# Performance work log

Measured on AMD Instinct MI355X. Metric: run time of the kernel, lower is better.

The kernel has to match this reference:

```python
import jax, jax.numpy as jnp
import numpy as np

B, S, DIN, DIM, H = 2, 2304, 1024, 1024, 16
HEAD_DIM = DIM // H            # 64
ROT_DIM = HEAD_DIM             # partial_rotary_factor = 1
BASE = 10000.0
EPS = 1e-6


def setup_inputs() -> dict:
    key = jax.random.key(0)
    ks = jax.random.split(key, 6)
    return {
        "input": jax.random.normal(ks[0], (B, S, DIN), dtype=jnp.float32),
        "qkv_w": jax.random.normal(ks[1], (3 * DIM, DIN), dtype=jnp.float32) * 0.02,
        "qkv_b": jnp.zeros((3 * DIM,), dtype=jnp.float32),
        "q_scale": jnp.ones((DIM,), dtype=jnp.float32),
        "k_scale": jnp.ones((DIM,), dtype=jnp.float32),
        "proj_w": jax.random.normal(ks[2], (DIN, DIM), dtype=jnp.float32) * 0.02,
        "proj_b": jnp.zeros((DIN,), dtype=jnp.float32),
        "height": 48,
        "width": 48,
    }


def _rms_norm(x, scale):
    # RMSNorm over the full inner dim (QKNorm), learned scale
    var = jnp.mean(x * x, axis=-1, keepdims=True)
    return x * jax.lax.rsqrt(var + EPS) * scale


def _rope_1d(x, pos):
    # x: (b, n, h, d_ax), pos: (n,) float; rotate_half-style RoPE
    d = x.shape[-1]
    inv_freq = 1.0 / (BASE ** (jnp.arange(0, d, 2, dtype=jnp.float32) / d))  # (d/2,)
    ang = pos[:, None] * inv_freq                                            # (n, d/2)
    cos = jnp.concatenate([jnp.cos(ang), jnp.cos(ang)], axis=-1)[None, :, None, :]
    sin = jnp.concatenate([jnp.sin(ang), jnp.sin(ang)], axis=-1)[None, :, None, :]
    x1, x2 = jnp.split(x, 2, axis=-1)
    rot = jnp.concatenate([-x2, x1], axis=-1)
    return x * cos + rot * sin


def _rope_2d(x, height, width):
    # axial 2D RoPE: first half of rotary dims keyed by row, second half by col
    n = height * width
    idx = jnp.arange(n, dtype=jnp.float32)
    rows = jnp.floor(idx / width)
    cols = jnp.mod(idx, width)
    half = ROT_DIM // 2
    x_r = _rope_1d(x[..., :half], rows)
    x_c = _rope_1d(x[..., half:ROT_DIM], cols)
    return jnp.concatenate([x_r, x_c, x[..., ROT_DIM:]], axis=-1)


def reference(input, qkv_w, qkv_b, q_scale, k_scale, proj_w, proj_b, height, width):
    b, n, _ = input.shape
    qkv = input @ qkv_w.T + qkv_b                       # (b, n, 3*dim)
    q, k, v = jnp.split(qkv, 3, axis=-1)
    q = _rms_norm(q, q_scale)
    k = _rms_norm(k, k_scale)
    # (b, n, h, d)
    q = q.reshape(b, n, H, HEAD_DIM)
    k = k.reshape(b, n, H, HEAD_DIM)
    v = v.reshape(b, n, H, HEAD_DIM)
    q = _rope_2d(q, height, width)
    k = _rope_2d(k, height, width)
    scale = HEAD_DIM ** (-0.5)
    # (b, h, q, k)
    scores = jnp.einsum("bqhd,bkhd->bhqk", q, k) * scale
    attn = jax.nn.softmax(scores, axis=-1)
    out = jnp.einsum("bhqk,bkhd->bqhd", attn, v)        # (b, n, h, d)
    out = out.reshape(b, n, DIM)
    return out @ proj_w.T + proj_b
```

## Files before the change

### kernel.cpp

```cpp
#include <hip/hip_runtime.h>
#include <math.h>

#define BB   2
#define SS   2304
#define DINC 1024
#define DIMC 1024
#define HH   16
#define HD   64

typedef _Float16 half_t;
typedef __attribute__((ext_vector_type(4))) _Float16 half4;
typedef __attribute__((ext_vector_type(8))) _Float16 half8;
typedef __attribute__((ext_vector_type(4))) float    f32x4;

#define LOG2E 1.44269504088896340736f
#define EXP2(x) __builtin_amdgcn_exp2f(x)

__device__ __forceinline__ half4 lo4(half8 x) { return (half4){x[0], x[1], x[2], x[3]}; }
__device__ __forceinline__ half4 hi4(half8 x) { return (half4){x[4], x[5], x[6], x[7]}; }

#define GLOAD_LDS16(gp, lp)                                                     \
    __builtin_amdgcn_global_load_lds(                                           \
        (const __attribute__((address_space(1))) void*)(gp),                    \
        (__attribute__((address_space(3))) void*)(lp), 16, 0, 0)

template<int RB>
__global__ __launch_bounds__(256)
void convert_tile_f16(const float* __restrict__ src, half_t* __restrict__ dst, int K)
{
    constexpr int EPT = RB * 32 / 256;
    const int mb = blockIdx.x;
    const int kb = blockIdx.y;
    const int t  = threadIdx.x;
    const int e0 = t * EPT;
    const int mm = e0 >> 5;
    const int kk = e0 & 31;
    const float* sp = src + (size_t)(mb * RB + mm) * K + kb * 32 + kk;
    half_t*      dp = dst + ((size_t)mb * (K >> 5) + kb) * (RB * 32) + mm * 32 + kk;
    #pragma unroll
    for (int g = 0; g < EPT / 4; ++g) {
        float4 v = *(const float4*)(sp + 4 * g);
        dp[4 * g + 0] = (half_t)v.x; dp[4 * g + 1] = (half_t)v.y;
        dp[4 * g + 2] = (half_t)v.z; dp[4 * g + 3] = (half_t)v.w;
    }
}

template<int BN, bool OUT_HALF>
__global__ __launch_bounds__(256)
void gemm_mfma(const half_t* __restrict__ Ah, const half_t* __restrict__ Bh,
               const float* __restrict__ bias, void* __restrict__ Cout,
               int M, int N, int K)
{
    constexpr int MT = (BN == 128) ? 4 : 2;
    constexpr int NT = 4;
    const int KB = K >> 5;
    __shared__ half_t As[8192];
    __shared__ half_t Bs[2 * BN * 32];

    const int t    = threadIdx.x;
    const int w    = t >> 6;
    const int lane = t & 63;
    const int l15  = lane & 15, quad = lane >> 4;
    const int wr   = (BN == 128) ? (w >> 1) : w;
    const int wc   = (BN == 128) ? (w & 1) : 0;
    const int mb   = blockIdx.y, nb = blockIdx.x;

    f32x4 acc[MT][NT];
    #pragma unroll
    for (int mt = 0; mt < MT; ++mt)
        #pragma unroll
        for (int nt = 0; nt < NT; ++nt) acc[mt][nt] = (f32x4){0.f, 0.f, 0.f, 0.f};

    const half_t* atile = Ah + (size_t)mb * KB * 4096;
    const half_t* btile = Bh + (size_t)nb * KB * (BN * 32);

    for (int kb = 0; kb < KB; kb += 2) {
        #pragma unroll
        for (int u = 0; u < 2; ++u) {
            const half_t* at = atile + (size_t)(kb + u) * 4096;
            const half_t* bt = btile + (size_t)(kb + u) * (BN * 32);
            #pragma unroll
            for (int v = 0; v < 2; ++v) {
                const int ch = w * 2 + v;
                GLOAD_LDS16(at + ch * 512 + lane * 8, As + u * 4096 + ch * 512);
            }
            if (BN == 128) {
                #pragma unroll
                for (int v = 0; v < 2; ++v) {
                    const int ch = w * 2 + v;
                    GLOAD_LDS16(bt + ch * 512 + lane * 8, Bs + u * 4096 + ch * 512);
                }
            } else {
                GLOAD_LDS16(bt + w * 512 + lane * 8, Bs + u * (BN * 32) + w * 512);
            }
        }
        __syncthreads();

        #pragma unroll
        for (int u = 0; u < 2; ++u) {
            half8 af[MT], bf[NT];
            #pragma unroll
            for (int mt = 0; mt < MT; ++mt)
                af[mt] = *(const half8*)(As + u * 4096
                                         + (wr * (MT * 16) + mt * 16 + l15) * 32 + quad * 8);
            #pragma unroll
            for (int nt = 0; nt < NT; ++nt)
                bf[nt] = *(const half8*)(Bs + u * (BN * 32)
                                         + (wc * 64 + nt * 16 + l15) * 32 + quad * 8);
            #pragma unroll
            for (int mt = 0; mt < MT; ++mt)
                #pragma unroll
                for (int nt = 0; nt < NT; ++nt)
                    acc[mt][nt] = __builtin_amdgcn_mfma_f32_16x16x32_f16(
                        af[mt], bf[nt], acc[mt][nt], 0, 0, 0);
        }
        __syncthreads();
    }

    const int bm = mb * 128, bn = nb * BN;
    #pragma unroll
    for (int nt = 0; nt < NT; ++nt) {
        const int n  = bn + wc * 64 + nt * 16 + l15;
        const float bv = bias[n];
        #pragma unroll
        for (int mt = 0; mt < MT; ++mt) {
            const int m0 = bm + wr * (MT * 16) + mt * 16 + quad * 4;
            #pragma unroll
            for (int rg = 0; rg < 4; ++rg) {
                const float v = acc[mt][nt][rg] + bv;
                if (OUT_HALF) ((half_t*)Cout)[(size_t)(m0 + rg) * N + n] = (half_t)v;
                else          ((float*) Cout)[(size_t)(m0 + rg) * N + n] = v;
            }
        }
    }
}

__global__ __launch_bounds__(256)
void normrope_v6(half_t* __restrict__ qkvh, const float* __restrict__ q_scale,
                 const float* __restrict__ k_scale, const int* __restrict__ wptr,
                 half_t* __restrict__ Kf, half_t* __restrict__ Vf)
{
    const int token = blockIdx.x;
    const int s     = token % SS;
    const int b     = token / SS;
    const int w     = *wptr;
    const int t     = threadIdx.x;
    const float rowp = (float)(s / w);
    const float colp = (float)(s % w);

    half_t* base = qkvh + (size_t)token * 3072;

    const int fr = s >> 5;
    const int jt = (s >> 4) & 1;

    {
        half4 v4 = *(const half4*)(base + 2048 + 4 * t);
        const int dabs0 = 4 * t;
        const int h  = dabs0 >> 6;
        const int vq = (s & 15) >> 2;
        const int vi = s & 3;
        half_t* vdst = Vf + ((size_t)(b * HH + h) * 72 + fr) * 2048 + jt * 1024;
        #pragma unroll
        for (int ii = 0; ii < 4; ++ii) {
            const int d   = (dabs0 + ii) & 63;
            const int dt  = d >> 4;
            vdst[(size_t)(dt >> 1) * 512 + ((d & 15) + 16 * vq) * 8 + (dt & 1) * 4 + vi]
                = v4[ii];
        }
    }

    __shared__ float buf[DIMC];
    __shared__ float red[4];

    const int km = s & 15;

    #pragma unroll
    for (int sel = 0; sel < 2; ++sel) {
        half_t* row = base + sel * DIMC;
        const float* scp = sel ? k_scale : q_scale;

        half4 xh = *(const half4*)(row + 4 * t);
        float x0 = (float)xh[0], x1 = (float)xh[1], x2 = (float)xh[2], x3 = (float)xh[3];
        float ss = x0 * x0 + x1 * x1 + x2 * x2 + x3 * x3;
        #pragma unroll
        for (int o = 32; o >= 1; o >>= 1) ss += __shfl_xor(ss, o);
        if ((t & 63) == 0) red[t >> 6] = ss;
        __syncthreads();

        const float rinv = rsqrtf((red[0] + red[1] + red[2] + red[3]) * (1.0f / DIMC) + 1e-6f);
        float4 g = *(const float4*)(scp + 4 * t);
        buf[4 * t + 0] = x0 * rinv * g.x;
        buf[4 * t + 1] = x1 * rinv * g.y;
        buf[4 * t + 2] = x2 * rinv * g.z;
        buf[4 * t + 3] = x3 * rinv * g.w;
        __syncthreads();

        const float qsc = sel ? 1.0f : (0.125f * LOG2E);

        #pragma unroll
        for (int pp = 0; pp < 2; ++pp) {
            const int p = t + pp * 256;
            const int h = p >> 5;
            const int r = p & 31;
            const int j = r & 15;
            const float pos = (r < 16) ? rowp : colp;
            const int d1 = (r < 16) ? j : (32 + j);
            const int d2 = d1 + 16;
            const float freq = exp2f((float)j * -0.83048202372f);
            const float ang  = pos * freq;
            float sn, cs;
            __sincosf(ang, &sn, &cs);
            const float a1 = buf[h * HD + d1], a2 = buf[h * HD + d2];
            const float o1 = (a1 * cs - a2 * sn) * qsc;
            const float o2 = (a2 * cs + a1 * sn) * qsc;
            if (sel == 0) {
                row[h * HD + d1] = (half_t)o1;
                row[h * HD + d2] = (half_t)o2;
            } else {
                half_t* kdst = Kf + ((size_t)(b * HH + h) * 72 + fr) * 2048 + jt * 1024;
                kdst[(size_t)(d1 >> 5) * 512 + (km + 16 * ((d1 & 31) >> 3)) * 8 + (d1 & 7)]
                    = (half_t)o1;
                kdst[(size_t)(d2 >> 5) * 512 + (km + 16 * ((d2 & 31) >> 3)) * 8 + (d2 & 7)]
                    = (half_t)o2;
            }
        }
        __syncthreads();
    }
}

__global__ __launch_bounds__(256, 4)
void flash_attn_mfma6(const half_t* __restrict__ qkvh, const half_t* __restrict__ Kf,
                      const half_t* __restrict__ Vf, half_t* __restrict__ attn_h)
{
    const int flat = blockIdx.x;
    const int xcd  = flat & 7;
    const int jj   = flat >> 3;
    const int bh   = xcd * 4 + (jj / 36);
    const int qtb  = jj % 36;
    const int b    = bh >> 4, h = bh & 15;
    const int t    = threadIdx.x;
    const int w    = t >> 6;
    const int jt   = w & 1;
    const int qh   = w >> 1;
    const int lane = t & 63;
    const int l15  = lane & 15, quad = lane >> 4;

    const size_t tb = (size_t)b * SS;
    const int q0 = qtb * 64;

    __shared__ float mlb[4][32][2];
    __shared__ float Ob[2][64][33];

    half8 qf[2][2];
    #pragma unroll
    for (int qt = 0; qt < 2; ++qt)
        #pragma unroll
        for (int dt2 = 0; dt2 < 2; ++dt2)
            qf[qt][dt2] = *(const half8*)(qkvh + (tb + q0 + qh * 32 + qt * 16 + l15) * 3072
                                          + h * HD + dt2 * 32 + quad * 8);

    f32x4 acc[4][2];
    float m_i[2], l_i[2];
    #pragma unroll
    for (int qt = 0; qt < 2; ++qt) {
        m_i[qt] = -INFINITY; l_i[qt] = 0.f;
        #pragma unroll
        for (int dt = 0; dt < 4; ++dt) acc[dt][qt] = (f32x4){0.f, 0.f, 0.f, 0.f};
    }

    const half_t* kpl = Kf + (size_t)bh * 72 * 2048 + jt * 1024 + lane * 8;
    const half_t* vpl = Vf + (size_t)bh * 72 * 2048 + jt * 1024 + lane * 8;

    auto step = [&](half8 kf0, half8 kf1, half8 v01, half8 v23) {
        half4 vf[4] = {lo4(v01), hi4(v01), lo4(v23), hi4(v23)};
        f32x4 sc[2];
        #pragma unroll
        for (int qt = 0; qt < 2; ++qt) {
            sc[qt] = (f32x4){0.f, 0.f, 0.f, 0.f};
            sc[qt] = __builtin_amdgcn_mfma_f32_16x16x32_f16(kf0, qf[qt][0], sc[qt], 0, 0, 0);
            sc[qt] = __builtin_amdgcn_mfma_f32_16x16x32_f16(kf1, qf[qt][1], sc[qt], 0, 0, 0);
        }
        half4 pf[2];
        #pragma unroll
        for (int qt = 0; qt < 2; ++qt) {
            float mx = fmaxf(fmaxf(sc[qt][0], sc[qt][1]), fmaxf(sc[qt][2], sc[qt][3]));
            mx = fmaxf(mx, __shfl_xor(mx, 16));
            mx = fmaxf(mx, __shfl_xor(mx, 32));
            if (__any(mx > m_i[qt])) {
                const float mn = fmaxf(m_i[qt], mx);
                const float alpha = EXP2(m_i[qt] - mn);
                m_i[qt] = mn;
                l_i[qt] *= alpha;
                #pragma unroll
                for (int dt = 0; dt < 4; ++dt) acc[dt][qt] *= alpha;
            }
            const float m = m_i[qt];
            const float p0 = EXP2(sc[qt][0] - m);
            const float p1 = EXP2(sc[qt][1] - m);
            const float p2 = EXP2(sc[qt][2] - m);
            const float p3 = EXP2(sc[qt][3] - m);
            l_i[qt] += (p0 + p1) + (p2 + p3);
            pf[qt] = (half4){(half_t)p0, (half_t)p1, (half_t)p2, (half_t)p3};
        }
        #pragma unroll
        for (int dt = 0; dt < 4; ++dt)
            #pragma unroll
            for (int qt = 0; qt < 2; ++qt)
                acc[dt][qt] = __builtin_amdgcn_mfma_f32_16x16x16f16(
                    vf[dt], pf[qt], acc[dt][qt], 0, 0, 0);
    };

    half8 kA0 = *(const half8*)(kpl);
    half8 kA1 = *(const half8*)(kpl + 512);
    half8 vA0 = *(const half8*)(vpl);
    half8 vA1 = *(const half8*)(vpl + 512);

    for (int fr2 = 0; fr2 < 36; ++fr2) {
        const int fr = fr2 * 2;
        const half_t* kB = kpl + (size_t)(fr + 1) * 2048;
        const half_t* vB = vpl + (size_t)(fr + 1) * 2048;
        half8 kB0 = *(const half8*)(kB);
        half8 kB1 = *(const half8*)(kB + 512);
        half8 vB0 = *(const half8*)(vB);
        half8 vB1 = *(const half8*)(vB + 512);

        step(kA0, kA1, vA0, vA1);

        if (fr + 2 < 72) {
            const half_t* kA = kpl + (size_t)(fr + 2) * 2048;
            const half_t* vA = vpl + (size_t)(fr + 2) * 2048;
            kA0 = *(const half8*)(kA);
            kA1 = *(const half8*)(kA + 512);
            vA0 = *(const half8*)(vA);
            vA1 = *(const half8*)(vA + 512);
        }

        step(kB0, kB1, vB0, vB1);
    }

    #pragma unroll
    for (int qt = 0; qt < 2; ++qt) {
        float lq = l_i[qt];
        lq += __shfl_xor(lq, 16);
        lq += __shfl_xor(lq, 32);
        if (quad == 0) {
            mlb[w][qt * 16 + l15][0] = m_i[qt];
            mlb[w][qt * 16 + l15][1] = lq;
        }
    }
    __syncthreads();

    float fac[2];
    #pragma unroll
    for (int qt = 0; qt < 2; ++qt) {
        const int q = qt * 16 + l15;
        const float m0 = mlb[qh * 2 + 0][q][0], m1 = mlb[qh * 2 + 1][q][0];
        const float M  = fmaxf(m0, m1);
        const float L  = mlb[qh * 2 + 0][q][1] * EXP2(m0 - M)
                       + mlb[qh * 2 + 1][q][1] * EXP2(m1 - M);
        fac[qt] = EXP2(m_i[qt] - M) / L;
    }

    #pragma unroll
    for (int ph = 0; ph < 2; ++ph) {
        if (jt == ph) {
            #pragma unroll
            for (int dt = 0; dt < 4; ++dt)
                #pragma unroll
                for (int qt = 0; qt < 2; ++qt)
                    #pragma unroll
                    for (int rg = 0; rg < 4; ++rg) {
                        const int d = dt * 16 + quad * 4 + rg;
                        const int q = qt * 16 + l15;
                        const float v = acc[dt][qt][rg] * fac[qt];
                        if (ph == 0) Ob[qh][d][q] = v;
                        else         Ob[qh][d][q] += v;
                    }
        }
        __syncthreads();
    }

    {
        const int q   = t >> 2;
        const int ds  = (t & 3) * 16;
        const int qh2 = q >> 5, qq = q & 31;
        const size_t mrow = tb + q0 + q;
        const int mb2 = (int)(mrow >> 7);
        const int mm  = (int)(mrow & 127);
        #pragma unroll
        for (int g = 0; g < 4; ++g) {
            const int dd = ds + 4 * g;
            const int kb2 = (h * HD + dd) >> 5;
            const int kk  = dd & 31;
            half4 o;
            o[0] = (half_t)Ob[qh2][dd + 0][qq];
            o[1] = (half_t)Ob[qh2][dd + 1][qq];
            o[2] = (half_t)Ob[qh2][dd + 2][qq];
            o[3] = (half_t)Ob[qh2][dd + 3][qq];
            *(half4*)(attn_h + ((size_t)mb2 * 32 + kb2) * 4096 + mm * 32 + kk) = o;
        }
    }
}

extern "C" void kernel_launch(void* const* d_in, const int* in_sizes, int n_in,
                              void* d_out, int out_size, void* d_ws, size_t ws_size,
                              hipStream_t stream)
{
    const float* input   = (const float*)d_in[0];
    const float* qkv_w   = (const float*)d_in[1];
    const float* qkv_b   = (const float*)d_in[2];
    const float* q_scale = (const float*)d_in[3];
    const float* k_scale = (const float*)d_in[4];
    const float* proj_w  = (const float*)d_in[5];
    const float* proj_b  = (const float*)d_in[6];
    const int*   width   = (const int*)d_in[8];
    float* out = (float*)d_out;

    half_t* qkvh   = (half_t*)d_ws;
    half_t* attn_h = qkvh   + (size_t)4608 * 3072;
    half_t* Vf     = attn_h + (size_t)4608 * 1024;
    half_t* Ah     = Vf     + (size_t)32 * 72 * 2048;
    half_t* Bh1    = Ah     + (size_t)4608 * 1024;
    half_t* Bh2    = Bh1    + (size_t)3072 * 1024;
    half_t* Kf     = Ah;

    const int M = BB * SS;

    convert_tile_f16<128><<<dim3(M / 128, DINC / 32),        256, 0, stream>>>(input,  Ah,  DINC);
    convert_tile_f16<128><<<dim3(3 * DIMC / 128, DINC / 32), 256, 0, stream>>>(qkv_w, Bh1, DINC);
    convert_tile_f16<64><<<dim3(DINC / 64, DIMC / 32),       256, 0, stream>>>(proj_w, Bh2, DIMC);

    gemm_mfma<128, true><<<dim3(3 * DIMC / 128, M / 128), 256, 0, stream>>>(
        Ah, Bh1, qkv_b, qkvh, M, 3 * DIMC, DINC);

    normrope_v6<<<M, 256, 0, stream>>>(qkvh, q_scale, k_scale, width, Kf, Vf);

    flash_attn_mfma6<<<dim3(SS / 64 * BB * HH), 256, 0, stream>>>(qkvh, Kf, Vf, attn_h);

    gemm_mfma<64, false><<<dim3(DINC / 64, M / 128), 256, 0, stream>>>(
        attn_h, Bh2, proj_b, out, M, DINC, DIMC);
}
```

Baseline: 271.0 us.

## Process two key tiles per softmax step and use 16x16x32 MFMA for PV

The K/V pre-layout in the norm/RoPE kernel is reorganised so each attention step handles 32 keys per wave. The score max, rescale and exp work is amortised over two 16-key tiles, and the PV product uses the wider 16x16x32 f16 MFMA in place of the 16x16x16 one. The norm/RoPE kernel now runs Q and K normalisation in parallel within a single 512-thread block, with no sequential loop. The cost is more live registers in the attention step, which may pressure occupancy at launch bound 4.

```diff
diff --git a/kernel.cpp b/kernel.cpp
--- a/kernel.cpp
+++ b/kernel.cpp
@@ -15,9 +15,6 @@
 
 #define LOG2E 1.44269504088896340736f
 #define EXP2(x) __builtin_amdgcn_exp2f(x)
-
-__device__ __forceinline__ half4 lo4(half8 x) { return (half4){x[0], x[1], x[2], x[3]}; }
-__device__ __forceinline__ half4 hi4(half8 x) { return (half4){x[4], x[5], x[6], x[7]}; }
 
 #define GLOAD_LDS16(gp, lp)                                                     \
     __builtin_amdgcn_global_load_lds(                                           \
@@ -135,8 +132,8 @@
     }
 }
 
-__global__ __launch_bounds__(256)
-void normrope_v6(half_t* __restrict__ qkvh, const float* __restrict__ q_scale,
+__global__ __launch_bounds__(512)
+void normrope_v7(half_t* __restrict__ qkvh, const float* __restrict__ q_scale,
                  const float* __restrict__ k_scale, const int* __restrict__ wptr,
                  half_t* __restrict__ Kf, half_t* __restrict__ Vf)
 {
@@ -150,86 +147,84 @@
 
     half_t* base = qkvh + (size_t)token * 3072;
 
-    const int fr = s >> 5;
-    const int jt = (s >> 4) & 1;
+    const int g36 = s >> 6;
+    const int jt  = (s >> 4) & 1;
+    const int kp_ = ((s >> 5) & 1) * 16 + (s & 15);
 
     {
-        half4 v4 = *(const half4*)(base + 2048 + 4 * t);
-        const int dabs0 = 4 * t;
-        const int h  = dabs0 >> 6;
-        const int vq = (s & 15) >> 2;
-        const int vi = s & 3;
-        half_t* vdst = Vf + ((size_t)(b * HH + h) * 72 + fr) * 2048 + jt * 1024;
-        #pragma unroll
-        for (int ii = 0; ii < 4; ++ii) {
-            const int d   = (dabs0 + ii) & 63;
-            const int dt  = d >> 4;
-            vdst[(size_t)(dt >> 1) * 512 + ((d & 15) + 16 * vq) * 8 + (dt & 1) * 4 + vi]
-                = v4[ii];
-        }
-    }
-
-    __shared__ float buf[DIMC];
-    __shared__ float red[4];
-
-    const int km = s & 15;
-
-    #pragma unroll
-    for (int sel = 0; sel < 2; ++sel) {
-        half_t* row = base + sel * DIMC;
-        const float* scp = sel ? k_scale : q_scale;
-
-        half4 xh = *(const half4*)(row + 4 * t);
-        float x0 = (float)xh[0], x1 = (float)xh[1], x2 = (float)xh[2], x3 = (float)xh[3];
-        float ss = x0 * x0 + x1 * x1 + x2 * x2 + x3 * x3;
-        #pragma unroll
-        for (int o = 32; o >= 1; o >>= 1) ss += __shfl_xor(ss, o);
-        if ((t & 63) == 0) red[t >> 6] = ss;
-        __syncthreads();
-
-        const float rinv = rsqrtf((red[0] + red[1] + red[2] + red[3]) * (1.0f / DIMC) + 1e-6f);
-        float4 g = *(const float4*)(scp + 4 * t);
-        buf[4 * t + 0] = x0 * rinv * g.x;
-        buf[4 * t + 1] = x1 * rinv * g.y;
-        buf[4 * t + 2] = x2 * rinv * g.z;
-        buf[4 * t + 3] = x3 * rinv * g.w;
-        __syncthreads();
-
-        const float qsc = sel ? 1.0f : (0.125f * LOG2E);
-
-        #pragma unroll
-        for (int pp = 0; pp < 2; ++pp) {
-            const int p = t + pp * 256;
-            const int h = p >> 5;
-            const int r = p & 31;
-            const int j = r & 15;
-            const float pos = (r < 16) ? rowp : colp;
-            const int d1 = (r < 16) ? j : (32 + j);
-            const int d2 = d1 + 16;
-            const float freq = exp2f((float)j * -0.83048202372f);
-            const float ang  = pos * freq;
-            float sn, cs;
-            __sincosf(ang, &sn, &cs);
-            const float a1 = buf[h * HD + d1], a2 = buf[h * HD + d2];
-            const float o1 = (a1 * cs - a2 * sn) * qsc;
-            const float o2 = (a2 * cs + a1 * sn) * qsc;
-            if (sel == 0) {
-                row[h * HD + d1] = (half_t)o1;
-                row[h * HD + d2] = (half_t)o2;
-            } else {
-                half_t* kdst = Kf + ((size_t)(b * HH + h) * 72 + fr) * 2048 + jt * 1024;
-                kdst[(size_t)(d1 >> 5) * 512 + (km + 16 * ((d1 & 31) >> 3)) * 8 + (d1 & 7)]
-                    = (half_t)o1;
-                kdst[(size_t)(d2 >> 5) * 512 + (km + 16 * ((d2 & 31) >> 3)) * 8 + (d2 & 7)]
-                    = (half_t)o2;
-            }
-        }
-        __syncthreads();
+        const int e0 = 2 * t;
+        const int kq = kp_ >> 3, ki = kp_ & 7;
+        #pragma unroll
+        for (int ii = 0; ii < 2; ++ii) {
+            const int e = e0 + ii;
+            const int h = e >> 6;
+            const int d = e & 63;
+            half_t* vdst = Vf + (((size_t)(b * HH + h) * 36 + g36) * 2 + jt) * 2048;
+            vdst[(size_t)(d >> 4) * 512 + ((d & 15) + 16 * kq) * 8 + ki] = base[2048 + e];
+        }
+    }
+
+    __shared__ float buf[2][DIMC];
+    __shared__ float red[8];
+
+    const int sel = t >> 8;
+    const int tl  = t & 255;
+    half_t* row = base + sel * DIMC;
+    const float* scp = sel ? k_scale : q_scale;
+
+    half4 xh = *(const half4*)(row + 4 * tl);
+    float x0 = (float)xh[0], x1 = (float)xh[1], x2 = (float)xh[2], x3 = (float)xh[3];
+    float ss = x0 * x0 + x1 * x1 + x2 * x2 + x3 * x3;
+    #pragma unroll
+    for (int o = 32; o >= 1; o >>= 1) ss += __shfl_xor(ss, o);
+    if ((tl & 63) == 0) red[sel * 4 + (tl >> 6)] = ss;
+    __syncthreads();
+
+    const float rinv = rsqrtf((red[sel * 4 + 0] + red[sel * 4 + 1]
+                             + red[sel * 4 + 2] + red[sel * 4 + 3]) * (1.0f / DIMC) + 1e-6f);
+    float4 g = *(const float4*)(scp + 4 * tl);
+    buf[sel][4 * tl + 0] = x0 * rinv * g.x;
+    buf[sel][4 * tl + 1] = x1 * rinv * g.y;
+    buf[sel][4 * tl + 2] = x2 * rinv * g.z;
+    buf[sel][4 * tl + 3] = x3 * rinv * g.w;
+    __syncthreads();
+
+    const float qsc = sel ? 1.0f : (0.125f * LOG2E);
+    const int ktile = (kp_ >> 2) & 1;
+    const int km    = ((kp_ >> 3) << 2) + (kp_ & 3);
+
+    #pragma unroll
+    for (int pp = 0; pp < 2; ++pp) {
+        const int p = tl + pp * 256;
+        const int h = p >> 5;
+        const int r = p & 31;
+        const int j = r & 15;
+        const float pos = (r < 16) ? rowp : colp;
+        const int d1 = (r < 16) ? j : (32 + j);
+        const int d2 = d1 + 16;
+        const float freq = exp2f((float)j * -0.83048202372f);
+        const float ang  = pos * freq;
+        float sn, cs;
+        __sincosf(ang, &sn, &cs);
+        const float a1 = buf[sel][h * HD + d1], a2 = buf[sel][h * HD + d2];
+        const float o1 = (a1 * cs - a2 * sn) * qsc;
+        const float o2 = (a2 * cs + a1 * sn) * qsc;
+        if (sel == 0) {
+            row[h * HD + d1] = (half_t)o1;
+            row[h * HD + d2] = (half_t)o2;
+        } else {
+            half_t* kdst = Kf + (((size_t)(b * HH + h) * 36 + g36) * 2 + jt) * 2048
+                         + ktile * 1024;
+            kdst[(size_t)(d1 >> 5) * 512 + (km + 16 * ((d1 & 31) >> 3)) * 8 + (d1 & 7)]
+                = (half_t)o1;
+            kdst[(size_t)(d2 >> 5) * 512 + (km + 16 * ((d2 & 31) >> 3)) * 8 + (d2 & 7)]
+                = (half_t)o2;
+        }
     }
 }
 
 __global__ __launch_bounds__(256, 4)
-void flash_attn_mfma6(const half_t* __restrict__ qkvh, const half_t* __restrict__ Kf,
+void flash_attn_mfma7(const half_t* __restrict__ qkvh, const half_t* __restrict__ Kf,
                       const half_t* __restrict__ Vf, half_t* __restrict__ attn_h)
 {
     const int flat = blockIdx.x;
@@ -268,22 +263,28 @@
         for (int dt = 0; dt < 4; ++dt) acc[dt][qt] = (f32x4){0.f, 0.f, 0.f, 0.f};
     }
 
-    const half_t* kpl = Kf + (size_t)bh * 72 * 2048 + jt * 1024 + lane * 8;
-    const half_t* vpl = Vf + (size_t)bh * 72 * 2048 + jt * 1024 + lane * 8;
-
-    auto step = [&](half8 kf0, half8 kf1, half8 v01, half8 v23) {
-        half4 vf[4] = {lo4(v01), hi4(v01), lo4(v23), hi4(v23)};
-        f32x4 sc[2];
+    const half_t* kpl = Kf + (((size_t)bh * 36) * 2 + jt) * 2048 + lane * 8;
+    const half_t* vpl = Vf + (((size_t)bh * 36) * 2 + jt) * 2048 + lane * 8;
+
+    auto step = [&](half8 kA0, half8 kA1, half8 kB0, half8 kB1,
+                    half8 v0, half8 v1, half8 v2, half8 v3) {
+        f32x4 scA[2], scB[2];
         #pragma unroll
         for (int qt = 0; qt < 2; ++qt) {
-            sc[qt] = (f32x4){0.f, 0.f, 0.f, 0.f};
-            sc[qt] = __builtin_amdgcn_mfma_f32_16x16x32_f16(kf0, qf[qt][0], sc[qt], 0, 0, 0);
-            sc[qt] = __builtin_amdgcn_mfma_f32_16x16x32_f16(kf1, qf[qt][1], sc[qt], 0, 0, 0);
-        }
-        half4 pf[2];
+            scA[qt] = (f32x4){0.f, 0.f, 0.f, 0.f};
+            scB[qt] = (f32x4){0.f, 0.f, 0.f, 0.f};
+            scA[qt] = __builtin_amdgcn_mfma_f32_16x16x32_f16(kA0, qf[qt][0], scA[qt], 0, 0, 0);
+            scA[qt] = __builtin_amdgcn_mfma_f32_16x16x32_f16(kA1, qf[qt][1], scA[qt], 0, 0, 0);
+            scB[qt] = __builtin_amdgcn_mfma_f32_16x16x32_f16(kB0, qf[qt][0], scB[qt], 0, 0, 0);
+            scB[qt] = __builtin_amdgcn_mfma_f32_16x16x32_f16(kB1, qf[qt][1], scB[qt], 0, 0, 0);
+        }
+        half8 pf[2];
         #pragma unroll
         for (int qt = 0; qt < 2; ++qt) {
-            float mx = fmaxf(fmaxf(sc[qt][0], sc[qt][1]), fmaxf(sc[qt][2], sc[qt][3]));
+            float mx = fmaxf(fmaxf(fmaxf(scA[qt][0], scA[qt][1]),
+                                   fmaxf(scA[qt][2], scA[qt][3])),
+                             fmaxf(fmaxf(scB[qt][0], scB[qt][1]),
+                                   fmaxf(scB[qt][2], scB[qt][3])));
             mx = fmaxf(mx, __shfl_xor(mx, 16));
             mx = fmaxf(mx, __shfl_xor(mx, 32));
             if (__any(mx > m_i[qt])) {
@@ -295,47 +296,65 @@
                 for (int dt = 0; dt < 4; ++dt) acc[dt][qt] *= alpha;
             }
             const float m = m_i[qt];
-            const float p0 = EXP2(sc[qt][0] - m);
-            const float p1 = EXP2(sc[qt][1] - m);
-            const float p2 = EXP2(sc[qt][2] - m);
-            const float p3 = EXP2(sc[qt][3] - m);
-            l_i[qt] += (p0 + p1) + (p2 + p3);
-            pf[qt] = (half4){(half_t)p0, (half_t)p1, (half_t)p2, (half_t)p3};
-        }
+            const float pA0 = EXP2(scA[qt][0] - m);
+            const float pA1 = EXP2(scA[qt][1] - m);
+            const float pA2 = EXP2(scA[qt][2] - m);
+            const float pA3 = EXP2(scA[qt][3] - m);
+            const float pB0 = EXP2(scB[qt][0] - m);
+            const float pB1 = EXP2(scB[qt][1] - m);
+            const float pB2 = EXP2(scB[qt][2] - m);
+            const float pB3 = EXP2(scB[qt][3] - m);
+            l_i[qt] += ((pA0 + pA1) + (pA2 + pA3)) + ((pB0 + pB1) + (pB2 + pB3));
+            pf[qt] = (half8){(half_t)pA0, (half_t)pA1, (half_t)pA2, (half_t)pA3,
+                             (half_t)pB0, (half_t)pB1, (half_t)pB2, (half_t)pB3};
+        }
+        half8 vf[4] = {v0, v1, v2, v3};
         #pragma unroll
         for (int dt = 0; dt < 4; ++dt)
             #pragma unroll
             for (int qt = 0; qt < 2; ++qt)
-                acc[dt][qt] = __builtin_amdgcn_mfma_f32_16x16x16f16(
+                acc[dt][qt] = __builtin_amdgcn_mfma_f32_16x16x32_f16(
                     vf[dt], pf[qt], acc[dt][qt], 0, 0, 0);
     };
 
     half8 kA0 = *(const half8*)(kpl);
     half8 kA1 = *(const half8*)(kpl + 512);
-    half8 vA0 = *(const half8*)(vpl);
-    half8 vA1 = *(const half8*)(vpl + 512);
-
-    for (int fr2 = 0; fr2 < 36; ++fr2) {
-        const int fr = fr2 * 2;
-        const half_t* kB = kpl + (size_t)(fr + 1) * 2048;
-        const half_t* vB = vpl + (size_t)(fr + 1) * 2048;
-        half8 kB0 = *(const half8*)(kB);
-        half8 kB1 = *(const half8*)(kB + 512);
-        half8 vB0 = *(const half8*)(vB);
-        half8 vB1 = *(const half8*)(vB + 512);
-
-        step(kA0, kA1, vA0, vA1);
-
-        if (fr + 2 < 72) {
-            const half_t* kA = kpl + (size_t)(fr + 2) * 2048;
-            const half_t* vA = vpl + (size_t)(fr + 2) * 2048;
-            kA0 = *(const half8*)(kA);
-            kA1 = *(const half8*)(kA + 512);
-            vA0 = *(const half8*)(vA);
-            vA1 = *(const half8*)(vA + 512);
-        }
-
-        step(kB0, kB1, vB0, vB1);
+    half8 kB0 = *(const half8*)(kpl + 1024);
+    half8 kB1 = *(const half8*)(kpl + 1536);
+    half8 va0 = *(const half8*)(vpl);
+    half8 va1 = *(const half8*)(vpl + 512);
+    half8 va2 = *(const half8*)(vpl + 1024);
+    half8 va3 = *(const half8*)(vpl + 1536);
+
+    for (int g2 = 0; g2 < 18; ++g2) {
+        const int g = g2 * 2;
+        const half_t* kN = kpl + (size_t)(g + 1) * 4096;
+        const half_t* vN = vpl + (size_t)(g + 1) * 4096;
+        half8 nk0 = *(const half8*)(kN);
+        half8 nk1 = *(const half8*)(kN + 512);
+        half8 nk2 = *(const half8*)(kN + 1024);
+        half8 nk3 = *(const half8*)(kN + 1536);
+        half8 nv0 = *(const half8*)(vN);
+        half8 nv1 = *(const half8*)(vN + 512);
+        half8 nv2 = *(const half8*)(vN + 1024);
+        half8 nv3 = *(const half8*)(vN + 1536);
+
+        step(kA0, kA1, kB0, kB1, va0, va1, va2, va3);
+
+        if (g + 2 < 36) {
+            const half_t* kM = kpl + (size_t)(g + 2) * 4096;
+            const half_t* vM = vpl + (size_t)(g + 2) * 4096;
+            kA0 = *(const half8*)(kM);
+            kA1 = *(const half8*)(kM + 512);
+            kB0 = *(const half8*)(kM + 1024);
+            kB1 = *(const half8*)(kM + 1536);
+            va0 = *(const half8*)(vM);
+            va1 = *(const half8*)(vM + 512);
+            va2 = *(const half8*)(vM + 1024);
+            va3 = *(const half8*)(vM + 1536);
+        }
+
+        step(nk0, nk1, nk2, nk3, nv0, nv1, nv2, nv3);
     }
 
     #pragma unroll
@@ -419,7 +438,7 @@
     half_t* qkvh   = (half_t*)d_ws;
     half_t* attn_h = qkvh   + (size_t)4608 * 3072;
     half_t* Vf     = attn_h + (size_t)4608 * 1024;
-    half_t* Ah     = Vf     + (size_t)32 * 72 * 2048;
+    half_t* Ah     = Vf     + (size_t)32 * 36 * 2 * 2048;
     half_t* Bh1    = Ah     + (size_t)4608 * 1024;
     half_t* Bh2    = Bh1    + (size_t)3072 * 1024;
     half_t* Kf     = Ah;
@@ -433,9 +452,9 @@
     gemm_mfma<128, true><<<dim3(3 * DIMC / 128, M / 128), 256, 0, stream>>>(
         Ah, Bh1, qkv_b, qkvh, M, 3 * DIMC, DINC);
 
-    normrope_v6<<<M, 256, 0, stream>>>(qkvh, q_scale, k_scale, width, Kf, Vf);
-
-    flash_attn_mfma6<<<dim3(SS / 64 * BB * HH), 256, 0, stream>>>(qkvh, Kf, Vf, attn_h);
+    normrope_v7<<<M, 512, 0, stream>>>(qkvh, q_scale, k_scale, width, Kf, Vf);
+
+    flash_attn_mfma7<<<dim3(SS / 64 * BB * HH), 256, 0, stream>>>(qkvh, Kf, Vf, attn_h);
 
     gemm_mfma<64, false><<<dim3(DINC / 64, M / 128), 256, 0, stream>>>(
         attn_h, Bh2, proj_b, out, M, DINC, DIMC);
```

Measured after the change: 325.0 us. 1.2x slower.

## Process two key frames per online-softmax step and split K/V prefetch

Applied to the files above, without the earlier changes.

The attention inner loop now computes scores for two 16-key frames together and runs a single max/rescale update over 32 keys instead of one per frame. This halves the cross-lane shuffles and conditional rescales. The next K fragments are prefetched right after the QK MFMAs, and the next V fragments after the PV MFMAs, so loads overlap with the softmax and matmul work. The cost is more live registers (two score sets and four K/V fragment pairs), which could lower occupancy under the 4-block launch bound.

```diff
diff --git a/kernel.cpp b/kernel.cpp
--- a/kernel.cpp
+++ b/kernel.cpp
@@ -229,7 +229,7 @@
 }
 
 __global__ __launch_bounds__(256, 4)
-void flash_attn_mfma6(const half_t* __restrict__ qkvh, const half_t* __restrict__ Kf,
+void flash_attn_mfma8(const half_t* __restrict__ qkvh, const half_t* __restrict__ Kf,
                       const half_t* __restrict__ Vf, half_t* __restrict__ attn_h)
 {
     const int flat = blockIdx.x;
@@ -271,19 +271,42 @@
     const half_t* kpl = Kf + (size_t)bh * 72 * 2048 + jt * 1024 + lane * 8;
     const half_t* vpl = Vf + (size_t)bh * 72 * 2048 + jt * 1024 + lane * 8;
 
-    auto step = [&](half8 kf0, half8 kf1, half8 v01, half8 v23) {
-        half4 vf[4] = {lo4(v01), hi4(v01), lo4(v23), hi4(v23)};
-        f32x4 sc[2];
+    half8 kA0 = *(const half8*)(kpl);
+    half8 kA1 = *(const half8*)(kpl + 512);
+    half8 kB0 = *(const half8*)(kpl + 2048);
+    half8 kB1 = *(const half8*)(kpl + 2560);
+    half8 vA0 = *(const half8*)(vpl);
+    half8 vA1 = *(const half8*)(vpl + 512);
+    half8 vB0 = *(const half8*)(vpl + 2048);
+    half8 vB1 = *(const half8*)(vpl + 2560);
+
+    for (int p = 0; p < 36; ++p) {
+        f32x4 scA[2], scB[2];
         #pragma unroll
         for (int qt = 0; qt < 2; ++qt) {
-            sc[qt] = (f32x4){0.f, 0.f, 0.f, 0.f};
-            sc[qt] = __builtin_amdgcn_mfma_f32_16x16x32_f16(kf0, qf[qt][0], sc[qt], 0, 0, 0);
-            sc[qt] = __builtin_amdgcn_mfma_f32_16x16x32_f16(kf1, qf[qt][1], sc[qt], 0, 0, 0);
-        }
-        half4 pf[2];
+            scA[qt] = (f32x4){0.f, 0.f, 0.f, 0.f};
+            scA[qt] = __builtin_amdgcn_mfma_f32_16x16x32_f16(kA0, qf[qt][0], scA[qt], 0, 0, 0);
+            scA[qt] = __builtin_amdgcn_mfma_f32_16x16x32_f16(kA1, qf[qt][1], scA[qt], 0, 0, 0);
+            scB[qt] = (f32x4){0.f, 0.f, 0.f, 0.f};
+            scB[qt] = __builtin_amdgcn_mfma_f32_16x16x32_f16(kB0, qf[qt][0], scB[qt], 0, 0, 0);
+            scB[qt] = __builtin_amdgcn_mfma_f32_16x16x32_f16(kB1, qf[qt][1], scB[qt], 0, 0, 0);
+        }
+
+        if (p + 1 < 36) {
+            const half_t* kN = kpl + (size_t)(p + 1) * 4096;
+            kA0 = *(const half8*)(kN);
+            kA1 = *(const half8*)(kN + 512);
+            kB0 = *(const half8*)(kN + 2048);
+            kB1 = *(const half8*)(kN + 2560);
+        }
+
+        half4 pfA[2], pfB[2];
         #pragma unroll
         for (int qt = 0; qt < 2; ++qt) {
-            float mx = fmaxf(fmaxf(sc[qt][0], sc[qt][1]), fmaxf(sc[qt][2], sc[qt][3]));
+            float mx = fmaxf(fmaxf(fmaxf(scA[qt][0], scA[qt][1]),
+                                   fmaxf(scA[qt][2], scA[qt][3])),
+                             fmaxf(fmaxf(scB[qt][0], scB[qt][1]),
+                                   fmaxf(scB[qt][2], scB[qt][3])));
             mx = fmaxf(mx, __shfl_xor(mx, 16));
             mx = fmaxf(mx, __shfl_xor(mx, 32));
             if (__any(mx > m_i[qt])) {
@@ -295,47 +318,38 @@
                 for (int dt = 0; dt < 4; ++dt) acc[dt][qt] *= alpha;
             }
             const float m = m_i[qt];
-            const float p0 = EXP2(sc[qt][0] - m);
-            const float p1 = EXP2(sc[qt][1] - m);
-            const float p2 = EXP2(sc[qt][2] - m);
-            const float p3 = EXP2(sc[qt][3] - m);
-            l_i[qt] += (p0 + p1) + (p2 + p3);
-            pf[qt] = (half4){(half_t)p0, (half_t)p1, (half_t)p2, (half_t)p3};
-        }
+            const float a0 = EXP2(scA[qt][0] - m);
+            const float a1 = EXP2(scA[qt][1] - m);
+            const float a2 = EXP2(scA[qt][2] - m);
+            const float a3 = EXP2(scA[qt][3] - m);
+            const float b0 = EXP2(scB[qt][0] - m);
+            const float b1 = EXP2(scB[qt][1] - m);
+            const float b2 = EXP2(scB[qt][2] - m);
+            const float b3 = EXP2(scB[qt][3] - m);
+            l_i[qt] += ((a0 + a1) + (a2 + a3)) + ((b0 + b1) + (b2 + b3));
+            pfA[qt] = (half4){(half_t)a0, (half_t)a1, (half_t)a2, (half_t)a3};
+            pfB[qt] = (half4){(half_t)b0, (half_t)b1, (half_t)b2, (half_t)b3};
+        }
+
+        half4 vfA[4] = {lo4(vA0), hi4(vA0), lo4(vA1), hi4(vA1)};
+        half4 vfB[4] = {lo4(vB0), hi4(vB0), lo4(vB1), hi4(vB1)};
         #pragma unroll
         for (int dt = 0; dt < 4; ++dt)
             #pragma unroll
-            for (int qt = 0; qt < 2; ++qt)
+            for (int qt = 0; qt < 2; ++qt) {
                 acc[dt][qt] = __builtin_amdgcn_mfma_f32_16x16x16f16(
-                    vf[dt], pf[qt], acc[dt][qt], 0, 0, 0);
-    };
-
-    half8 kA0 = *(const half8*)(kpl);
-    half8 kA1 = *(const half8*)(kpl + 512);
-    half8 vA0 = *(const half8*)(vpl);
-    half8 vA1 = *(const half8*)(vpl + 512);
-
-    for (int fr2 = 0; fr2 < 36; ++fr2) {
-        const int fr = fr2 * 2;
-        const half_t* kB = kpl + (size_t)(fr + 1) * 2048;
-        const half_t* vB = vpl + (size_t)(fr + 1) * 2048;
-        half8 kB0 = *(const half8*)(kB);
-        half8 kB1 = *(const half8*)(kB + 512);
-        half8 vB0 = *(const half8*)(vB);
-        half8 vB1 = *(const half8*)(vB + 512);
-
-        step(kA0, kA1, vA0, vA1);
-
-        if (fr + 2 < 72) {
-            const half_t* kA = kpl + (size_t)(fr + 2) * 2048;
-            const half_t* vA = vpl + (size_t)(fr + 2) * 2048;
-            kA0 = *(const half8*)(kA);
-            kA1 = *(const half8*)(kA + 512);
-            vA0 = *(const half8*)(vA);
-            vA1 = *(const half8*)(vA + 512);
-        }
-
-        step(kB0, kB1, vB0, vB1);
+                    vfA[dt], pfA[qt], acc[dt][qt], 0, 0, 0);
+                acc[dt][qt] = __builtin_amdgcn_mfma_f32_16x16x16f16(
+                    vfB[dt], pfB[qt], acc[dt][qt], 0, 0, 0);
+            }
+
+        if (p + 1 < 36) {
+            const half_t* vN = vpl + (size_t)(p + 1) * 4096;
+            vA0 = *(const half8*)(vN);
+            vA1 = *(const half8*)(vN + 512);
+            vB0 = *(const half8*)(vN + 2048);
+            vB1 = *(const half8*)(vN + 2560);
+        }
     }
 
     #pragma unroll
@@ -435,7 +449,7 @@
 
     normrope_v6<<<M, 256, 0, stream>>>(qkvh, q_scale, k_scale, width, Kf, Vf);
 
-    flash_attn_mfma6<<<dim3(SS / 64 * BB * HH), 256, 0, stream>>>(qkvh, Kf, Vf, attn_h);
+    flash_attn_mfma8<<<dim3(SS / 64 * BB * HH), 256, 0, stream>>>(qkvh, Kf, Vf, attn_h);
 
     gemm_mfma<64, false><<<dim3(DINC / 64, M / 128), 256, 0, stream>>>(
         attn_h, Bh2, proj_b, out, M, DINC, DIMC);
```

After: 266.0 us. Within noise of the previous version (-1.8%).
